# Kernel tuning notes

Hardware: AMD Instinct MI355X
Metric: run time of the kernel (lower is better)

## Reference

```python
import jax, jax.numpy as jnp
import numpy as np

N_CLS = 7  # only the first 7 channels contribute to the loss

def setup_inputs() -> dict:
    key = jax.random.key(0)
    k1, k2 = jax.random.split(key)
    pred = jax.random.normal(k1, (256, 16384, 8), dtype=jnp.float32)
    gt = jax.random.normal(k2, (256, 16384, 8), dtype=jnp.float32)
    return {"pred": pred, "gt": gt}

def reference(pred, gt):
    # per-batch loss: sum over objects and first 7 channels of squared error
    diff = pred[..., :N_CLS] - gt[..., :N_CLS]  # [B, N, 7]
    return jnp.sum(diff * diff, axis=(1, 2))    # [B]
```

## Files before the change

### kernel.cpp

```cpp
#include <hip/hip_runtime.h>


#define THREADS 256
#define SPLIT 8
#define F4_PER_BATCH (16384 * 2)
#define F4_PER_BLOCK (F4_PER_BATCH / SPLIT)
#define UNROLL 4
#define OUTER (F4_PER_BLOCK / (THREADS * UNROLL))

typedef float vfloat4 __attribute__((ext_vector_type(4)));

__global__ __launch_bounds__(THREADS) void label_loss_kernel(
    const vfloat4* __restrict__ pred,
    const vfloat4* __restrict__ gt,
    float* __restrict__ out)
{
    const int bx  = blockIdx.x;
    const int b   = bx / SPLIT;
    const int seg = bx % SPLIT;
    const long base = (long)b * F4_PER_BATCH + (long)seg * F4_PER_BLOCK;

    const float m = (threadIdx.x & 1) ? 0.0f : 1.0f;

    float acc0 = 0.0f, acc1 = 0.0f, acc2 = 0.0f, acc3 = 0.0f;

    #pragma unroll 1
    for (int it = 0; it < OUTER; ++it) {
        const long i0 = base + (long)it * (THREADS * UNROLL) + threadIdx.x;
        const vfloat4 p0 = __builtin_nontemporal_load(&pred[i0]);
        const vfloat4 p1 = __builtin_nontemporal_load(&pred[i0 + 256]);
        const vfloat4 p2 = __builtin_nontemporal_load(&pred[i0 + 512]);
        const vfloat4 p3 = __builtin_nontemporal_load(&pred[i0 + 768]);
        const vfloat4 g0 = gt[i0];
        const vfloat4 g1 = gt[i0 + 256];
        const vfloat4 g2 = gt[i0 + 512];
        const vfloat4 g3 = gt[i0 + 768];

        vfloat4 d;
        d = p0 - g0;
        acc0 += d.x * d.x + d.y * d.y + d.z * d.z + m * (d.w * d.w);
        d = p1 - g1;
        acc1 += d.x * d.x + d.y * d.y + d.z * d.z + m * (d.w * d.w);
        d = p2 - g2;
        acc2 += d.x * d.x + d.y * d.y + d.z * d.z + m * (d.w * d.w);
        d = p3 - g3;
        acc3 += d.x * d.x + d.y * d.y + d.z * d.z + m * (d.w * d.w);
    }

    float v = (acc0 + acc1) + (acc2 + acc3);

    #pragma unroll
    for (int off = 32; off > 0; off >>= 1)
        v += __shfl_down(v, off, 64);

    __shared__ float wsum[THREADS / 64];
    const int lane = threadIdx.x & 63;
    const int wave = threadIdx.x >> 6;
    if (lane == 0) wsum[wave] = v;
    __syncthreads();

    if (threadIdx.x == 0) {
        atomicAdd(&out[b], wsum[0] + wsum[1] + wsum[2] + wsum[3]);
    }
}

extern "C" void kernel_launch(void* const* d_in, const int* in_sizes, int n_in,
                              void* d_out, int out_size, void* d_ws, size_t ws_size,
                              hipStream_t stream) {
    const vfloat4* pred = (const vfloat4*)d_in[0];
    const vfloat4* gt   = (const vfloat4*)d_in[1];
    float* out = (float*)d_out;

    (void)hipMemsetAsync(d_out, 0, (size_t)out_size * sizeof(float), stream);

    const int n_blocks = 256 * SPLIT;
    label_loss_kernel<<<dim3(n_blocks), dim3(THREADS), 0, stream>>>(pred, gt, out);
}
```

Before: 261.4 us.

## Stage pred/gt loads through LDS via global_load_lds direct-to-shared copies

Replaces the direct register vector loads with global_load_lds instructions that copy pred and gt tiles straight into shared memory, then reads them back from LDS to compute squared differences. Each iteration now handles two rounds of 256 float4 per tensor, with two block barriers per iteration. The aim is to avoid passing loaded data through VGPRs on the way in, but it adds LDS traffic and barrier stalls and gives up the nontemporal hint and the 4-way unroll in flight.

```diff
diff --git a/kernel.cpp b/kernel.cpp
--- a/kernel.cpp
+++ b/kernel.cpp
@@ -1,65 +1,73 @@
 #include <hip/hip_runtime.h>
 
+
+typedef float vfloat4 __attribute__((ext_vector_type(4)));
 
 #define THREADS 256
 #define SPLIT 8
 #define F4_PER_BATCH (16384 * 2)
 #define F4_PER_BLOCK (F4_PER_BATCH / SPLIT)
-#define UNROLL 4
-#define OUTER (F4_PER_BLOCK / (THREADS * UNROLL))
-
-typedef float vfloat4 __attribute__((ext_vector_type(4)));
+#define ROUNDS 2
+#define F4_PER_ITER (THREADS * ROUNDS)
+#define NITER (F4_PER_BLOCK / F4_PER_ITER)
 
 __global__ __launch_bounds__(THREADS) void label_loss_kernel(
     const vfloat4* __restrict__ pred,
     const vfloat4* __restrict__ gt,
     float* __restrict__ out)
 {
-    const int bx  = blockIdx.x;
-    const int b   = bx / SPLIT;
-    const int seg = bx % SPLIT;
+    __shared__ vfloat4 sP[F4_PER_ITER];
+    __shared__ vfloat4 sG[F4_PER_ITER];
+
+    const int b   = blockIdx.x / SPLIT;
+    const int seg = blockIdx.x % SPLIT;
     const long base = (long)b * F4_PER_BATCH + (long)seg * F4_PER_BLOCK;
 
-    const float m = (threadIdx.x & 1) ? 0.0f : 1.0f;
+    const int tid   = threadIdx.x;
+    const int wbase = tid & ~63;
+    const float m = (tid & 1) ? 0.0f : 1.0f;
 
-    float acc0 = 0.0f, acc1 = 0.0f, acc2 = 0.0f, acc3 = 0.0f;
+    float acc0 = 0.0f, acc1 = 0.0f;
 
     #pragma unroll 1
-    for (int it = 0; it < OUTER; ++it) {
-        const long i0 = base + (long)it * (THREADS * UNROLL) + threadIdx.x;
-        const vfloat4 p0 = __builtin_nontemporal_load(&pred[i0]);
-        const vfloat4 p1 = __builtin_nontemporal_load(&pred[i0 + 256]);
-        const vfloat4 p2 = __builtin_nontemporal_load(&pred[i0 + 512]);
-        const vfloat4 p3 = __builtin_nontemporal_load(&pred[i0 + 768]);
-        const vfloat4 g0 = gt[i0];
-        const vfloat4 g1 = gt[i0 + 256];
-        const vfloat4 g2 = gt[i0 + 512];
-        const vfloat4 g3 = gt[i0 + 768];
+    for (int it = 0; it < NITER; ++it) {
+        const long g0 = base + (long)it * F4_PER_ITER;
 
-        vfloat4 d;
-        d = p0 - g0;
-        acc0 += d.x * d.x + d.y * d.y + d.z * d.z + m * (d.w * d.w);
-        d = p1 - g1;
-        acc1 += d.x * d.x + d.y * d.y + d.z * d.z + m * (d.w * d.w);
-        d = p2 - g2;
-        acc2 += d.x * d.x + d.y * d.y + d.z * d.z + m * (d.w * d.w);
-        d = p3 - g3;
-        acc3 += d.x * d.x + d.y * d.y + d.z * d.z + m * (d.w * d.w);
+        #pragma unroll
+        for (int r = 0; r < ROUNDS; ++r) {
+            __builtin_amdgcn_global_load_lds(
+                (const __attribute__((address_space(1))) void*)&pred[g0 + r * THREADS + tid],
+                (__attribute__((address_space(3))) void*)&sP[r * THREADS + wbase],
+                16, 0, 0);
+            __builtin_amdgcn_global_load_lds(
+                (const __attribute__((address_space(1))) void*)&gt[g0 + r * THREADS + tid],
+                (__attribute__((address_space(3))) void*)&sG[r * THREADS + wbase],
+                16, 0, 0);
+        }
+        __syncthreads();
+
+        {
+            const vfloat4 d0 = sP[tid] - sG[tid];
+            const vfloat4 d1 = sP[THREADS + tid] - sG[THREADS + tid];
+            acc0 += d0.x * d0.x + d0.y * d0.y + d0.z * d0.z + m * (d0.w * d0.w);
+            acc1 += d1.x * d1.x + d1.y * d1.y + d1.z * d1.z + m * (d1.w * d1.w);
+        }
+        __syncthreads();
     }
 
-    float v = (acc0 + acc1) + (acc2 + acc3);
+    float v = acc0 + acc1;
 
     #pragma unroll
     for (int off = 32; off > 0; off >>= 1)
         v += __shfl_down(v, off, 64);
 
     __shared__ float wsum[THREADS / 64];
-    const int lane = threadIdx.x & 63;
-    const int wave = threadIdx.x >> 6;
+    const int lane = tid & 63;
+    const int wave = tid >> 6;
     if (lane == 0) wsum[wave] = v;
     __syncthreads();
 
-    if (threadIdx.x == 0) {
+    if (tid == 0) {
         atomicAdd(&out[b], wsum[0] + wsum[1] + wsum[2] + wsum[3]);
     }
 }
```

After: 277.3 us. 1.06x slower.
